# Kernel optimization log

Measured on AMD Instinct MI355X. Metric: run time of the kernel, lower is better.

## Reference

```python
import jax, jax.numpy as jnp
import numpy as np

ALPHA = 0.25          # VQLayer commitment weight
KL_WEIGHT = 0.01      # settings.kl_weight (repo global)
ENTROPY_WEIGHT = 0.1  # settings.entropy_weight (repo global)


def _forward(x, W0, b0, W1, b1, Wmu, bmu, Wvar, bvar, protos, eps):
    # MLP encoder: input_dim -> 64 -> output_dim, relu after each layer
    h = jax.nn.relu(x @ W0.T + b0)
    h = jax.nn.relu(h @ W1.T + b1)
    logvar = h @ Wvar.T + bvar
    mu = h @ Wmu.T + bmu
    # reparameterize
    latents = mu + eps * jnp.exp(0.5 * logvar)  # [B, D]

    # squared euclidean distances to prototypes: [B, P]
    dists = (jnp.sum(latents ** 2, axis=1, keepdims=True)
             + jnp.sum(protos ** 2, axis=1)
             - 2.0 * latents @ protos.T)
    idx = jnp.argmin(dists, axis=1)              # [B]
    quantized = protos[idx]                      # == one_hot @ protos

    commitment_loss = jnp.mean((jax.lax.stop_gradient(quantized) - latents) ** 2)
    embedding_loss = jnp.mean((quantized - jax.lax.stop_gradient(latents)) ** 2)
    vq_loss = commitment_loss * ALPHA + embedding_loss

    # categorical entropy of mean soft assignment
    logdist = jax.nn.log_softmax(-dists, axis=1)
    soft_dist = jnp.mean(jnp.exp(logdist), axis=0) + 1e-6
    soft_dist = soft_dist / jnp.sum(soft_dist)
    ent = jnp.sum(-soft_dist * jnp.log(soft_dist))
    vq_loss = vq_loss + ENTROPY_WEIGHT * ent

    # straight-through estimator
    quantized = latents + jax.lax.stop_gradient(quantized - latents)

    divergence = jnp.mean(-0.5 * jnp.sum(1.0 + logvar - mu ** 2 - jnp.exp(logvar), axis=1))
    total_loss = KL_WEIGHT * divergence + vq_loss
    return quantized, total_loss, divergence


def setup_inputs() -> dict:
    key = jax.random.key(0)
    ks = jax.random.split(key, 12)
    B, IN, HID, D, P = 32768, 1024, 64, 512, 2048

    def lin(k, fan_in, fan_out):
        bound = 1.0 / np.sqrt(fan_in)
        k1, k2 = jax.random.split(k)
        W = jax.random.uniform(k1, (fan_out, fan_in), jnp.float32, -bound, bound)
        b = jax.random.uniform(k2, (fan_out,), jnp.float32, -bound, bound)
        return W, b

    W0, b0 = lin(ks[0], IN, HID)
    W1, b1 = lin(ks[1], HID, D)
    Wmu, bmu = lin(ks[2], D, D)
    Wvar, bvar = lin(ks[3], D, D)
    protos = jax.random.uniform(ks[4], (P, D), jnp.float32, -1.0 / P, 1.0 / P)
    x = jax.random.normal(ks[5], (B, IN), jnp.float32)
    eps = jax.random.normal(ks[6], (B, D), jnp.float32)
    return {"x": x, "W0": W0, "b0": b0, "W1": W1, "b1": b1,
            "Wmu": Wmu, "bmu": bmu, "Wvar": Wvar, "bvar": bvar,
            "protos": protos, "eps": eps}


def reference(x, W0, b0, W1, b1, Wmu, bmu, Wvar, bvar, protos, eps):
    return _forward(x, W0, b0, W1, b1, Wmu, bmu, Wvar, bvar, protos, eps)
```

## Files before the change

kernel.cpp:

```cpp
#include <hip/hip_runtime.h>
#include <math.h>

#define B_N 32768
#define IN_DIM 1024
#define HID 64
#define D_DIM 512
#define P_N 2048

typedef __attribute__((ext_vector_type(8))) short s16x8;
typedef __attribute__((ext_vector_type(4))) float f32x4;

__device__ __forceinline__ unsigned short f2bf(float f) {
    unsigned u = __float_as_uint(f);
    return (unsigned short)((u + 0x7fffu + ((u >> 16) & 1u)) >> 16);
}
__device__ __forceinline__ float bf2f(unsigned short v) {
    return __uint_as_float(((unsigned)v) << 16);
}

__device__ __forceinline__ void gl_lds(const void* gsrc, void* ldst) {
    __builtin_amdgcn_global_load_lds(
        (const __attribute__((address_space(1))) unsigned int*)gsrc,
        (__attribute__((address_space(3))) unsigned int*)ldst, 16, 0, 0);
}

__device__ __forceinline__ s16x8 pack8(const float* s) {
    float4 x = *(const float4*)s;
    float4 y = *(const float4*)(s + 4);
    s16x8 o;
    o[0] = (short)f2bf(x.x); o[1] = (short)f2bf(x.y);
    o[2] = (short)f2bf(x.z); o[3] = (short)f2bf(x.w);
    o[4] = (short)f2bf(y.x); o[5] = (short)f2bf(y.y);
    o[6] = (short)f2bf(y.z); o[7] = (short)f2bf(y.w);
    return o;
}

__global__ __launch_bounds__(256) void k_prep(const float* __restrict__ protos,
                                              const float* __restrict__ Wmu,
                                              const float* __restrict__ Wvar,
                                              const float* __restrict__ W0,
                                              const float* __restrict__ W1,
                                              unsigned short* __restrict__ pb16,
                                              float* __restrict__ pnorm,
                                              unsigned short* __restrict__ wmv16,
                                              unsigned short* __restrict__ w0pack,
                                              unsigned short* __restrict__ w1pack) {
    int gid = blockIdx.x * 256 + threadIdx.x;
    if (gid < 131072) {
        int row = gid >> 6, k8 = gid & 63;
        const float* s = protos + (size_t)row * 512 + k8 * 8;
        float4 x = *(const float4*)s;
        float4 y = *(const float4*)(s + 4);
        s16x8 o;
        o[0] = (short)f2bf(x.x); o[1] = (short)f2bf(x.y);
        o[2] = (short)f2bf(x.z); o[3] = (short)f2bf(x.w);
        o[4] = (short)f2bf(y.x); o[5] = (short)f2bf(y.y);
        o[6] = (short)f2bf(y.z); o[7] = (short)f2bf(y.w);
        ((s16x8*)pb16)[(size_t)row * 64 + k8] = o;
        float ss = x.x * x.x + x.y * x.y + x.z * x.z + x.w * x.w +
                   y.x * y.x + y.y * y.y + y.z * y.z + y.w * y.w;
#pragma unroll
        for (int d = 1; d < 64; d <<= 1) ss += __shfl_xor(ss, d);
        if ((threadIdx.x & 63) == 0) pnorm[row] = ss;
    } else if (gid < 196608) {
        int a = gid - 131072;
        int row = a >> 6, k8 = a & 63;
        int g = row >> 5, i = row & 31;
        const float* s = (i < 16 ? Wmu + (size_t)(g * 16 + i) * 512
                                 : Wvar + (size_t)(g * 16 + i - 16) * 512) + k8 * 8;
        ((s16x8*)wmv16)[(size_t)row * 64 + k8] = pack8(s);
    } else if (gid < 204800) {
        int a = gid - 196608;
        int row = a >> 7, k8 = a & 127;
        int K32 = k8 >> 2;
        int lane = (row & 15) | ((k8 & 3) << 4);
        ((s16x8*)w0pack)[((size_t)(row >> 4) * 32 + K32) * 64 + lane] =
            pack8(W0 + (size_t)row * IN_DIM + k8 * 8);
    } else {
        int a = gid - 204800;
        int row = a >> 3, k8 = a & 7;
        int K32 = k8 >> 2;
        int lane = (row & 15) | ((k8 & 3) << 4);
        ((s16x8*)w1pack)[((size_t)(row >> 4) * 2 + K32) * 64 + lane] =
            pack8(W1 + (size_t)row * HID + k8 * 8);
    }
}

__global__ __launch_bounds__(256, 4) void k_enc(const float* __restrict__ x,
                                                const unsigned short* __restrict__ w0p,
                                                const float* __restrict__ b0,
                                                const unsigned short* __restrict__ w1p,
                                                const float* __restrict__ b1,
                                                unsigned short* __restrict__ h2b) {
    __shared__ s16x8 As[1024];
    const int tid = threadIdx.x;
    const int l = tid & 63, wid = tid >> 6;
    const int bm = blockIdx.x * 64;
    const s16x8* w0p8 = (const s16x8*)w0p;
    const s16x8* w1p8 = (const s16x8*)w1p;

    const int srow = tid >> 2, ssub = tid & 3;
    const int srb = srow * 256, ssw = (srow & 7) << 4;
    const int klane = (l >> 4) << 4;
    const int sw = (l & 7) << 4;
    const int arow = wid * 16 + (l & 15);

    f32x4 acc1[4];
#pragma unroll
    for (int pf = 0; pf < 4; ++pf) acc1[pf] = (f32x4)0.f;

    for (int kt = 0; kt < 8; ++kt) {
        const float* src = x + (size_t)(bm + srow) * IN_DIM + kt * 128 + ssub * 32;
#pragma unroll
        for (int it = 0; it < 4; ++it) {
            s16x8 o = pack8(src + it * 8);
            int kbyte = ssub * 64 + it * 16;
            As[(srb + (kbyte ^ ssw)) >> 4] = o;
        }
        __syncthreads();
#pragma unroll
        for (int K32 = 0; K32 < 4; ++K32) {
            const int Kg = kt * 4 + K32;
            s16x8 b[4];
#pragma unroll
            for (int pf = 0; pf < 4; ++pf) b[pf] = w0p8[((size_t)pf * 32 + Kg) * 64 + l];
            s16x8 a = As[(arow * 256 + ((K32 * 64 + klane) ^ sw)) >> 4];
#pragma unroll
            for (int pf = 0; pf < 4; ++pf)
                acc1[pf] = __builtin_amdgcn_mfma_f32_16x16x32_bf16(a, b[pf], acc1[pf], 0, 0, 0);
        }
        __syncthreads();
    }

    {
        unsigned short* Hs = (unsigned short*)As;
#pragma unroll
        for (int pf = 0; pf < 4; ++pf) {
            const int c = pf * 16 + (l & 15);
            const float bb = b0[c];
#pragma unroll
            for (int j = 0; j < 4; ++j) {
                const int r = wid * 16 + (l >> 4) * 4 + j;
                float v = fmaxf(acc1[pf][j] + bb, 0.f);
                int byte = r * 128 + ((c * 2) ^ ((r & 7) << 4));
                Hs[byte >> 1] = f2bf(v);
            }
        }
    }
    __syncthreads();

    s16x8 a2[2];
#pragma unroll
    for (int K32 = 0; K32 < 2; ++K32)
        a2[K32] = As[(arow * 128 + ((K32 * 64 + klane) ^ sw)) >> 4];

    const int r0 = bm + wid * 16 + (l >> 4) * 4;
#pragma unroll
    for (int ct = 0; ct < 4; ++ct) {
        f32x4 acc2[8];
#pragma unroll
        for (int pf = 0; pf < 8; ++pf) acc2[pf] = (f32x4)0.f;
#pragma unroll
        for (int K32 = 0; K32 < 2; ++K32)
#pragma unroll
            for (int pf = 0; pf < 8; ++pf) {
                s16x8 b = w1p8[(((size_t)(ct * 8 + pf)) * 2 + K32) * 64 + l];
                acc2[pf] = __builtin_amdgcn_mfma_f32_16x16x32_bf16(a2[K32], b, acc2[pf], 0, 0, 0);
            }
#pragma unroll
        for (int pf = 0; pf < 8; ++pf) {
            const int c = ct * 128 + pf * 16 + (l & 15);
            const float bb = b1[c];
#pragma unroll
            for (int j = 0; j < 4; ++j)
                h2b[(size_t)(r0 + j) * D_DIM + c] = f2bf(fmaxf(acc2[pf][j] + bb, 0.f));
        }
    }
}

#define GEMM_CORE(Aptr, Bptr)                                                  \
    __shared__ s16x8 A8[1024];                                                 \
    __shared__ s16x8 B8[1024];                                                 \
    const int tid = threadIdx.x;                                               \
    const int l = tid & 63, w = tid >> 6;                                      \
    const int bm = blockIdx.x * 128;                                           \
    const int bn = blockIdx.y * 128;                                           \
    const int wr = w >> 1, wc = w & 1;                                         \
    const int srow = l >> 3;                                                   \
    const int scol = (((l & 7) ^ ((l >> 3) & 7)) * 8);                         \
    f32x4 acc[4][4];                                                           \
    _Pragma("unroll") for (int m = 0; m < 4; ++m)                              \
        _Pragma("unroll") for (int n = 0; n < 4; ++n) acc[m][n] = (f32x4)0.f;  \
    for (int kt = 0; kt < 8; ++kt) {                                           \
        __syncthreads();                                                       \
        _Pragma("unroll") for (int i = 0; i < 4; ++i) {                        \
            const int rb = w * 32 + i * 8;                                     \
            gl_lds(Aptr + (size_t)(bm + rb + srow) * 512 + kt * 64 + scol,     \
                   (char*)A8 + rb * 128);                                      \
            gl_lds(Bptr + (size_t)(bn + rb + srow) * 512 + kt * 64 + scol,     \
                   (char*)B8 + rb * 128);                                      \
        }                                                                      \
        __syncthreads();                                                       \
        _Pragma("unroll") for (int K32 = 0; K32 < 2; ++K32) {                  \
            const int kb = (K32 * 64 + (l >> 4) * 16) ^ ((l & 7) << 4);        \
            s16x8 a[4], b[4];                                                  \
            _Pragma("unroll") for (int m = 0; m < 4; ++m)                      \
                a[m] = A8[((wr * 64 + m * 16 + (l & 15)) * 128 + kb) >> 4];    \
            _Pragma("unroll") for (int n = 0; n < 4; ++n)                      \
                b[n] = B8[((wc * 64 + n * 16 + (l & 15)) * 128 + kb) >> 4];    \
            _Pragma("unroll") for (int m = 0; m < 4; ++m)                      \
                _Pragma("unroll") for (int n = 0; n < 4; ++n)                  \
                    acc[m][n] = __builtin_amdgcn_mfma_f32_16x16x32_bf16(       \
                        a[m], b[n], acc[m][n], 0, 0, 0);                       \
        }                                                                      \
    }

__global__ __launch_bounds__(256, 4) void k_mv(const unsigned short* __restrict__ h2b,
                                               const unsigned short* __restrict__ wmv16,
                                               const float* __restrict__ bmu,
                                               const float* __restrict__ bvar,
                                               const float* __restrict__ eps,
                                               unsigned short* __restrict__ lat16,
                                               float* __restrict__ div_acc) {
    GEMM_CORE(h2b, wmv16)
    __shared__ float red[4];
    float kl = 0.f;
    const int dbase0 = (bn >> 1) + wc * 32;
#pragma unroll
    for (int m = 0; m < 4; ++m)
#pragma unroll
        for (int nn = 0; nn < 2; ++nn) {
            const int d = dbase0 + nn * 16 + (l & 15);
            const float bmv = bmu[d], bvv = bvar[d];
#pragma unroll
            for (int j = 0; j < 4; ++j) {
                const int r = bm + wr * 64 + m * 16 + (l >> 4) * 4 + j;
                float mu = acc[m][2 * nn][j] + bmv;
                float lv = acc[m][2 * nn + 1][j] + bvv;
                float ev = __builtin_nontemporal_load(&eps[(size_t)r * D_DIM + d]);
                float la = fmaf(ev, __expf(0.5f * lv), mu);
                lat16[(size_t)r * D_DIM + d] = f2bf(la);
                kl += mu * mu + __expf(lv) - lv - 1.f;
            }
        }
    kl *= 0.5f;
#pragma unroll
    for (int d = 1; d < 64; d <<= 1) kl += __shfl_xor(kl, d);
    if (l == 0) red[w] = kl;
    __syncthreads();
    if (tid == 0) atomicAdd(div_acc, red[0] + red[1] + red[2] + red[3]);
}

__global__ __launch_bounds__(256, 4) void k_vq1(const unsigned short* __restrict__ lat16,
                                                const unsigned short* __restrict__ pb16,
                                                const float* __restrict__ pnorm,
                                                float* __restrict__ rowS,
                                                unsigned* __restrict__ rowKey,
                                                unsigned short* __restrict__ gA,
                                                unsigned short* __restrict__ gB) {
    GEMM_CORE(lat16, pb16)
    __shared__ float rowS_l[128];
    __shared__ unsigned rowKey_l[128];
    if (tid < 128) { rowS_l[tid] = 0.f; rowKey_l[tid] = 0u; }
    __syncthreads();
    float pn[4];
#pragma unroll
    for (int n = 0; n < 4; ++n) pn[n] = pnorm[bn + wc * 64 + n * 16 + (l & 15)];
    s16x8* gd8 = (s16x8*)((blockIdx.y < 8) ? gA : gB);
    const size_t gbase = ((size_t)((blockIdx.y & 7) * 256 + blockIdx.x) * 8) * 256;
#pragma unroll
    for (int m = 0; m < 4; ++m) {
        float gv[4][4], ev[4][4];
#pragma unroll
        for (int n = 0; n < 4; ++n)
#pragma unroll
            for (int j = 0; j < 4; ++j) {
                gv[n][j] = 2.f * acc[m][n][j] - pn[n];
                ev[n][j] = __expf(gv[n][j]);
            }
        s16x8 u0, u1;
#pragma unroll
        for (int j = 0; j < 4; ++j) {
            u0[j] = (short)f2bf(ev[0][j]); u0[4 + j] = (short)f2bf(ev[1][j]);
            u1[j] = (short)f2bf(ev[2][j]); u1[4 + j] = (short)f2bf(ev[3][j]);
        }
        __builtin_nontemporal_store(u0, &gd8[gbase + (size_t)(m * 2 + 0) * 256 + tid]);
        __builtin_nontemporal_store(u1, &gd8[gbase + (size_t)(m * 2 + 1) * 256 + tid]);
#pragma unroll
        for (int j = 0; j < 4; ++j) {
            float se = ev[0][j] + ev[1][j] + ev[2][j] + ev[3][j];
            unsigned key = 0u;
#pragma unroll
            for (int n = 0; n < 4; ++n) {
                const int p = bn + wc * 64 + n * 16 + (l & 15);
                unsigned kk = (__float_as_uint(gv[n][j] + 16.0f) & 0xFFFFF800u) | (unsigned)(2047 - p);
                key = key > kk ? key : kk;
            }
#pragma unroll
            for (int d = 1; d < 16; d <<= 1) {
                se += __shfl_xor(se, d);
                unsigned ok = (unsigned)__shfl_xor((int)key, d);
                key = key > ok ? key : ok;
            }
            if ((l & 15) == 0) {
                const int rloc = wr * 64 + m * 16 + (l >> 4) * 4 + j;
                atomicAdd(&rowS_l[rloc], se);
                atomicMax(&rowKey_l[rloc], key);
            }
        }
    }
    __syncthreads();
    if (tid < 128) {
        atomicAdd(&rowS[bm + tid], rowS_l[tid]);
        atomicMax(&rowKey[bm + tid], rowKey_l[tid]);
    }
}

__global__ __launch_bounds__(256, 4) void k_vq2s(const unsigned short* __restrict__ gA,
                                                 const unsigned short* __restrict__ gB,
                                                 const float* __restrict__ rowS,
                                                 float* __restrict__ soft_acc) {
    __shared__ float soft_l[128];
    const int tid = threadIdx.x;
    const int l = tid & 63, w = tid >> 6;
    const int wr = w >> 1, wc = w & 1;
    const int bm = blockIdx.x * 128;
    const int bn = blockIdx.y * 128;
    if (tid < 128) soft_l[tid] = 0.f;
    __syncthreads();

    const s16x8* gs8 = (const s16x8*)((blockIdx.y < 8) ? gA : gB);
    const size_t gbase = ((size_t)((blockIdx.y & 7) * 256 + blockIdx.x) * 8) * 256;

    float is[4][4];
#pragma unroll
    for (int m = 0; m < 4; ++m)
#pragma unroll
        for (int j = 0; j < 4; ++j)
            is[m][j] = 1.0f / rowS[bm + wr * 64 + m * 16 + (l >> 4) * 4 + j];

    float cs[4] = {0.f, 0.f, 0.f, 0.f};
#pragma unroll
    for (int m = 0; m < 4; ++m) {
        s16x8 u0 = __builtin_nontemporal_load(&gs8[gbase + (size_t)(m * 2 + 0) * 256 + tid]);
        s16x8 u1 = __builtin_nontemporal_load(&gs8[gbase + (size_t)(m * 2 + 1) * 256 + tid]);
#pragma unroll
        for (int j = 0; j < 4; ++j) {
            cs[0] += bf2f((unsigned short)u0[j]) * is[m][j];
            cs[1] += bf2f((unsigned short)u0[4 + j]) * is[m][j];
            cs[2] += bf2f((unsigned short)u1[j]) * is[m][j];
            cs[3] += bf2f((unsigned short)u1[4 + j]) * is[m][j];
        }
    }
#pragma unroll
    for (int n = 0; n < 4; ++n) {
        cs[n] += __shfl_xor(cs[n], 16);
        cs[n] += __shfl_xor(cs[n], 32);
    }
    if (l < 16) {
#pragma unroll
        for (int n = 0; n < 4; ++n) atomicAdd(&soft_l[wc * 64 + n * 16 + l], cs[n]);
    }
    __syncthreads();
    if (tid < 128) atomicAdd(&soft_acc[bn + tid], soft_l[tid]);
}

__global__ __launch_bounds__(256) void k_quant(const float* __restrict__ protos,
                                               const unsigned* __restrict__ rowKey,
                                               const unsigned short* __restrict__ lat16,
                                               float* __restrict__ out,
                                               float* __restrict__ vq_part) {
    const int tid = threadIdx.x;
    const int l = tid & 63, wid = tid >> 6;
    const int base = blockIdx.x * 64;
    float s = 0.f;
#pragma unroll
    for (int it = 0; it < 16; ++it) {
        const int r = base + it * 4 + wid;
        const int p = 2047 - (int)(rowKey[r] & 2047u);
        const float4* qp = (const float4*)(protos + (size_t)p * D_DIM);
        float4* op = (float4*)(out + (size_t)r * D_DIM);
        s16x8 lv = ((const s16x8*)(lat16 + (size_t)r * D_DIM))[l];
        float4 q1 = qp[l * 2], q2 = qp[l * 2 + 1];
        float d0 = q1.x - bf2f((unsigned short)lv[0]);
        float d1 = q1.y - bf2f((unsigned short)lv[1]);
        float d2 = q1.z - bf2f((unsigned short)lv[2]);
        float d3 = q1.w - bf2f((unsigned short)lv[3]);
        float d4 = q2.x - bf2f((unsigned short)lv[4]);
        float d5 = q2.y - bf2f((unsigned short)lv[5]);
        float d6 = q2.z - bf2f((unsigned short)lv[6]);
        float d7 = q2.w - bf2f((unsigned short)lv[7]);
        s += d0 * d0 + d1 * d1 + d2 * d2 + d3 * d3 +
             d4 * d4 + d5 * d5 + d6 * d6 + d7 * d7;
        op[l * 2] = q1; op[l * 2 + 1] = q2;
    }
#pragma unroll
    for (int m = 1; m < 64; m <<= 1) s += __shfl_xor(s, m);
    __shared__ float red[4];
    if (l == 0) red[wid] = s;
    __syncthreads();
    if (tid == 0) vq_part[blockIdx.x] = red[0] + red[1] + red[2] + red[3];
}

__global__ __launch_bounds__(256) void k_final(const float* __restrict__ soft_acc,
                                               const float* __restrict__ scal,
                                               const float* __restrict__ vq_part,
                                               float* __restrict__ out) {
    const int tid = threadIdx.x;
    __shared__ float red[256];
    float vals[8];
    float s = 0.f;
#pragma unroll
    for (int i = 0; i < 8; ++i) {
        float v = soft_acc[tid * 8 + i] * (1.0f / B_N) + 1e-6f;
        vals[i] = v;
        s += v;
    }
    red[tid] = s;
    __syncthreads();
    for (int off = 128; off > 0; off >>= 1) {
        if (tid < off) red[tid] += red[tid + off];
        __syncthreads();
    }
    float norm = red[0];
    __syncthreads();
    float e = 0.f;
#pragma unroll
    for (int i = 0; i < 8; ++i) {
        float p = vals[i] / norm;
        e -= p * __logf(p);
    }
    red[tid] = e;
    __syncthreads();
    for (int off = 128; off > 0; off >>= 1) {
        if (tid < off) red[tid] += red[tid + off];
        __syncthreads();
    }
    float ent = red[0];
    __syncthreads();
    red[tid] = vq_part[tid] + vq_part[tid + 256];
    __syncthreads();
    for (int off = 128; off > 0; off >>= 1) {
        if (tid < off) red[tid] += red[tid + off];
        __syncthreads();
    }
    if (tid == 0) {
        float div = scal[0] * (1.0f / B_N);
        float vq = red[0] * (1.0f / ((float)B_N * (float)D_DIM));
        float vq_loss = 1.25f * vq + 0.1f * ent;
        float total = 0.01f * div + vq_loss;
        out[(size_t)B_N * D_DIM] = total;
        out[(size_t)B_N * D_DIM + 1] = div;
    }
}

extern "C" void kernel_launch(void* const* d_in, const int* in_sizes, int n_in,
                              void* d_out, int out_size, void* d_ws, size_t ws_size,
                              hipStream_t stream) {
    const float* x = (const float*)d_in[0];
    const float* W0 = (const float*)d_in[1];
    const float* b0 = (const float*)d_in[2];
    const float* W1 = (const float*)d_in[3];
    const float* b1 = (const float*)d_in[4];
    const float* Wmu = (const float*)d_in[5];
    const float* bmu = (const float*)d_in[6];
    const float* Wvar = (const float*)d_in[7];
    const float* bvar = (const float*)d_in[8];
    const float* protos = (const float*)d_in[9];
    const float* eps = (const float*)d_in[10];
    float* out = (float*)d_out;

    unsigned short* wsp = (unsigned short*)d_ws;
    unsigned short* lat16 = wsp;
    unsigned short* pb16 = lat16 + (size_t)B_N * D_DIM;
    unsigned short* wmv16 = pb16 + (size_t)P_N * D_DIM;
    unsigned short* w0pack = wmv16 + (size_t)2 * D_DIM * D_DIM;
    unsigned short* w1pack = w0pack + (size_t)HID * IN_DIM;
    float* pnorm = (float*)(w1pack + (size_t)D_DIM * HID);
    float* rowS = pnorm + P_N;
    unsigned* rowKey = (unsigned*)(rowS + B_N);
    float* soft = (float*)(rowKey + B_N);
    float* scal = soft + P_N;
    float* vqpart = scal + 2;
    unsigned short* h2b = (unsigned short*)(vqpart + 512) +
                          (size_t)B_N * HID;
    unsigned short* gA = (unsigned short*)(vqpart + 512);
    unsigned short* gB = (unsigned short*)d_out;

    hipMemsetAsync(rowS, 0, (size_t)(B_N * 2 + P_N + 2) * 4, stream);

    k_prep<<<816, 256, 0, stream>>>(protos, Wmu, Wvar, W0, W1,
                                    pb16, pnorm, wmv16, w0pack, w1pack);

    k_enc<<<B_N / 64, 256, 0, stream>>>(x, w0pack, b0, w1pack, b1, h2b);

    dim3 gmv(B_N / 128, 8);
    k_mv<<<gmv, 256, 0, stream>>>(h2b, wmv16, bmu, bvar, eps, lat16, scal);

    dim3 gvq(B_N / 128, 16);
    k_vq1<<<gvq, 256, 0, stream>>>(lat16, pb16, pnorm, rowS, rowKey, gA, gB);
    k_vq2s<<<gvq, 256, 0, stream>>>(gA, gB, rowS, soft);

    k_quant<<<B_N / 64, 256, 0, stream>>>(protos, rowKey, lat16, out, vqpart);
    k_final<<<1, 256, 0, stream>>>(soft, scal, vqpart, out);
}
```

Measured before the change: 292.7 us.

## Derive VQ loss from row norms and argmin keys, drop latent reread in gather

Accumulates the sum of squared latents in k_mv alongside the KL term. k_final then recovers the total squared quantization error as that latent norm sum minus the per-row best-distance values decoded from the packed argmin keys, taken as ||q||^2 - 2 l·q with an offset of 16. As a result k_quant no longer reads the bf16 latents or reduces the error: it only gathers prototype rows and writes them with nontemporal stores. The trade-offs are precision loss from truncated key bits and from cancellation between two large sums, plus a serial 32K-element loop inside the single-block k_final.

```diff
diff --git a/kernel.cpp b/kernel.cpp
--- a/kernel.cpp
+++ b/kernel.cpp
@@ -221,10 +221,11 @@
                                                const float* __restrict__ bvar,
                                                const float* __restrict__ eps,
                                                unsigned short* __restrict__ lat16,
-                                               float* __restrict__ div_acc) {
+                                               float* __restrict__ scal) {
     GEMM_CORE(h2b, wmv16)
-    __shared__ float red[4];
-    float kl = 0.f;
+    __shared__ float redK[4];
+    __shared__ float redL[4];
+    float kl = 0.f, ln = 0.f;
     const int dbase0 = (bn >> 1) + wc * 32;
 #pragma unroll
     for (int m = 0; m < 4; ++m)
@@ -241,14 +242,21 @@
                 float la = fmaf(ev, __expf(0.5f * lv), mu);
                 lat16[(size_t)r * D_DIM + d] = f2bf(la);
                 kl += mu * mu + __expf(lv) - lv - 1.f;
+                ln += la * la;
             }
         }
     kl *= 0.5f;
 #pragma unroll
-    for (int d = 1; d < 64; d <<= 1) kl += __shfl_xor(kl, d);
-    if (l == 0) red[w] = kl;
-    __syncthreads();
-    if (tid == 0) atomicAdd(div_acc, red[0] + red[1] + red[2] + red[3]);
+    for (int d = 1; d < 64; d <<= 1) {
+        kl += __shfl_xor(kl, d);
+        ln += __shfl_xor(ln, d);
+    }
+    if (l == 0) { redK[w] = kl; redL[w] = ln; }
+    __syncthreads();
+    if (tid == 0) {
+        atomicAdd(&scal[0], redK[0] + redK[1] + redK[2] + redK[3]);
+        atomicAdd(&scal[1], redL[0] + redL[1] + redL[2] + redL[3]);
+    }
 }
 
 __global__ __launch_bounds__(256, 4) void k_vq1(const unsigned short* __restrict__ lat16,
@@ -367,44 +375,25 @@
 
 __global__ __launch_bounds__(256) void k_quant(const float* __restrict__ protos,
                                                const unsigned* __restrict__ rowKey,
-                                               const unsigned short* __restrict__ lat16,
-                                               float* __restrict__ out,
-                                               float* __restrict__ vq_part) {
+                                               float* __restrict__ out) {
     const int tid = threadIdx.x;
     const int l = tid & 63, wid = tid >> 6;
     const int base = blockIdx.x * 64;
-    float s = 0.f;
 #pragma unroll
     for (int it = 0; it < 16; ++it) {
         const int r = base + it * 4 + wid;
         const int p = 2047 - (int)(rowKey[r] & 2047u);
-        const float4* qp = (const float4*)(protos + (size_t)p * D_DIM);
-        float4* op = (float4*)(out + (size_t)r * D_DIM);
-        s16x8 lv = ((const s16x8*)(lat16 + (size_t)r * D_DIM))[l];
-        float4 q1 = qp[l * 2], q2 = qp[l * 2 + 1];
-        float d0 = q1.x - bf2f((unsigned short)lv[0]);
-        float d1 = q1.y - bf2f((unsigned short)lv[1]);
-        float d2 = q1.z - bf2f((unsigned short)lv[2]);
-        float d3 = q1.w - bf2f((unsigned short)lv[3]);
-        float d4 = q2.x - bf2f((unsigned short)lv[4]);
-        float d5 = q2.y - bf2f((unsigned short)lv[5]);
-        float d6 = q2.z - bf2f((unsigned short)lv[6]);
-        float d7 = q2.w - bf2f((unsigned short)lv[7]);
-        s += d0 * d0 + d1 * d1 + d2 * d2 + d3 * d3 +
-             d4 * d4 + d5 * d5 + d6 * d6 + d7 * d7;
-        op[l * 2] = q1; op[l * 2 + 1] = q2;
-    }
-#pragma unroll
-    for (int m = 1; m < 64; m <<= 1) s += __shfl_xor(s, m);
-    __shared__ float red[4];
-    if (l == 0) red[wid] = s;
-    __syncthreads();
-    if (tid == 0) vq_part[blockIdx.x] = red[0] + red[1] + red[2] + red[3];
+        const f32x4* qp = (const f32x4*)(protos + (size_t)p * D_DIM);
+        f32x4* op = (f32x4*)(out + (size_t)r * D_DIM);
+        f32x4 q1 = qp[l * 2], q2 = qp[l * 2 + 1];
+        __builtin_nontemporal_store(q1, &op[l * 2]);
+        __builtin_nontemporal_store(q2, &op[l * 2 + 1]);
+    }
 }
 
 __global__ __launch_bounds__(256) void k_final(const float* __restrict__ soft_acc,
                                                const float* __restrict__ scal,
-                                               const float* __restrict__ vq_part,
+                                               const unsigned* __restrict__ rowKey,
                                                float* __restrict__ out) {
     const int tid = threadIdx.x;
     __shared__ float red[256];
@@ -438,7 +427,12 @@
     }
     float ent = red[0];
     __syncthreads();
-    red[tid] = vq_part[tid] + vq_part[tid + 256];
+    float gsum = 0.f;
+    for (int i = 0; i < 128; ++i) {
+        unsigned k = rowKey[i * 256 + tid];
+        gsum += __uint_as_float(k & 0xFFFFF800u) - 16.0f;
+    }
+    red[tid] = gsum;
     __syncthreads();
     for (int off = 128; off > 0; off >>= 1) {
         if (tid < off) red[tid] += red[tid + off];
@@ -446,7 +440,7 @@
     }
     if (tid == 0) {
         float div = scal[0] * (1.0f / B_N);
-        float vq = red[0] * (1.0f / ((float)B_N * (float)D_DIM));
+        float vq = (scal[1] - red[0]) * (1.0f / ((float)B_N * (float)D_DIM));
         float vq_loss = 1.25f * vq + 0.1f * ent;
         float total = 0.01f * div + vq_loss;
         out[(size_t)B_N * D_DIM] = total;
@@ -481,10 +475,9 @@
     unsigned* rowKey = (unsigned*)(rowS + B_N);
     float* soft = (float*)(rowKey + B_N);
     float* scal = soft + P_N;
-    float* vqpart = scal + 2;
-    unsigned short* h2b = (unsigned short*)(vqpart + 512) +
+    unsigned short* h2b = (unsigned short*)(scal + 2 + 510) +
                           (size_t)B_N * HID;
-    unsigned short* gA = (unsigned short*)(vqpart + 512);
+    unsigned short* gA = (unsigned short*)(scal + 2 + 510);
     unsigned short* gB = (unsigned short*)d_out;
 
     hipMemsetAsync(rowS, 0, (size_t)(B_N * 2 + P_N + 2) * 4, stream);
@@ -501,6 +494,6 @@
     k_vq1<<<gvq, 256, 0, stream>>>(lat16, pb16, pnorm, rowS, rowKey, gA, gB);
     k_vq2s<<<gvq, 256, 0, stream>>>(gA, gB, rowS, soft);
 
-    k_quant<<<B_N / 64, 256, 0, stream>>>(protos, rowKey, lat16, out, vqpart);
-    k_final<<<1, 256, 0, stream>>>(soft, scal, vqpart, out);
-}
+    k_quant<<<B_N / 64, 256, 0, stream>>>(protos, rowKey, out);
+    k_final<<<1, 256, 0, stream>>>(soft, scal, rowKey, out);
+}
```

Result: slower. 310.6 us (+6.1%).
